# Kernel optimization log

Hardware: AMD Instinct MI355X
Metric: run time of the kernel (lower is better)

## Reference

```python
import jax, jax.numpy as jnp
import numpy as np

Z_DIM = 64
K = 2048
N = 32768


def setup_inputs() -> dict:
    key = jax.random.key(0)
    k1, k2 = jax.random.split(key)
    x = jax.random.normal(k1, (N, Z_DIM), dtype=jnp.float32)
    # init.normal_(locs, std=sqrt(z_dim))
    locs = jax.random.normal(k2, (K, Z_DIM), dtype=jnp.float32) * np.sqrt(Z_DIM)
    logits = jnp.zeros((K,), dtype=jnp.float32)  # maxent buffer
    return {"x": x, "locs": locs, "logits": logits}


def reference(x, locs, logits):
    d = x.shape[-1]
    var = jnp.float32(d)  # scale = sqrt(z_dim) -> variance = z_dim
    # squared distances [N, K] via cdist expansion (avoids [N,K,d] intermediate)
    sq = (
        jnp.sum(x * x, axis=-1, keepdims=True)
        + jnp.sum(locs * locs, axis=-1)[None, :]
        - 2.0 * (x @ locs.T)
    )
    # Independent Normal log prob summed over z_dim
    log_norm_const = d * (0.5 * jnp.log(2.0 * jnp.pi) + 0.5 * jnp.log(var))
    comp_log_prob = -0.5 * sq / var - log_norm_const  # [N, K]
    mix_logits = jax.nn.log_softmax(logits)  # Categorical normalizes logits
    wlp = comp_log_prob + mix_logits  # weighted_log_prob, [N, K]
    log_prob = jax.nn.logsumexp(wlp, axis=-1)  # [N]
    modes = jnp.argmax(wlp, axis=-1)  # assign_modes, [N]
    quantized = locs[modes]  # hard_quantize, [N, z_dim]
    return log_prob, quantized
```

## Files before the change

kernel.cpp:

```cpp
#include <hip/hip_runtime.h>
#include <math.h>

#define N_SAMP 32768
#define K_COMP 2048
#define ZD 64
#define LNC 191.896324792608546f
#define LN2F 0.69314718055994531f
#define INV_LN2 1.44269504088896340f
#define S2C 0.02254211001388974f

#define TILES_TOT 128
#define TPS 8
#define STAGES (TILES_TOT / TPS)
#define STAGE_B (TPS * 2048)

typedef __attribute__((ext_vector_type(8))) short short8;
typedef __attribute__((ext_vector_type(4))) float v4f;

#if __has_builtin(__builtin_amdgcn_exp2f)
#define EXP2(x) __builtin_amdgcn_exp2f(x)
#else
#define EXP2(x) exp2f(x)
#endif

typedef const __attribute__((address_space(1))) unsigned int* gas_t;
typedef __attribute__((address_space(3))) unsigned int* las_t;
__device__ inline void gload_lds16(const void* g, void* l) {
    __builtin_amdgcn_global_load_lds((gas_t)g, (las_t)l, 16, 0, 0);
}

__device__ inline unsigned short f2bf(float f) {
    unsigned int u = __float_as_uint(f);
    u += 0x7fffu + ((u >> 16) & 1u);
    return (unsigned short)(u >> 16);
}
__device__ inline float bf2f(unsigned short h) {
    return __uint_as_float(((unsigned int)h) << 16);
}
__device__ inline float med3f(float x, float y, float z) {
    return fmaxf(fminf(x, y), fminf(fmaxf(x, y), z));
}

__global__ __launch_bounds__(256) void prep_kernel(
    const float* __restrict__ locs, const float* __restrict__ logits,
    float* __restrict__ ck2, float* __restrict__ lse_out,
    char* __restrict__ lf) {
    if (blockIdx.x < 64) {
        int gid = blockIdx.x * 256 + threadIdx.x;
        int k = gid >> 3;
        int dc = gid & 7;
        int T = k >> 4, n = k & 15;

        const float* src = locs + (size_t)k * ZD + dc * 8;
        float4 u0 = *(const float4*)(src);
        float4 u1 = *(const float4*)(src + 4);
        float a[8] = {u0.x, u0.y, u0.z, u0.w, u1.x, u1.y, u1.z, u1.w};

        short8 h;
        float sq = 0.f;
#pragma unroll
        for (int j = 0; j < 8; ++j) {
            h[j] = (short)f2bf(a[j]);
            sq = fmaf(a[j], a[j], sq);
        }
        *(short8*)(lf + (size_t)T * 2048 + (dc >> 2) * 1024 +
                   ((size_t)(n + 16 * (dc & 3))) * 16) = h;

        sq += __shfl_xor(sq, 1);
        sq += __shfl_xor(sq, 2);
        sq += __shfl_xor(sq, 4);
        if (dc == 0) ck2[k] = (logits[k] - sq * (1.0f / 128.0f)) * INV_LN2;
    } else {
        __shared__ float red[4];
        int tid = threadIdx.x;
        int wv = tid >> 6, ln = tid & 63;
        float lm = -INFINITY;
        for (int i = tid; i < K_COMP; i += 256) lm = fmaxf(lm, logits[i]);
#pragma unroll
        for (int d = 1; d < 64; d <<= 1) lm = fmaxf(lm, __shfl_xor(lm, d));
        if (ln == 0) red[wv] = lm;
        __syncthreads();
        float M = fmaxf(fmaxf(red[0], red[1]), fmaxf(red[2], red[3]));
        float ls = 0.f;
        for (int i = tid; i < K_COMP; i += 256) ls += __expf(logits[i] - M);
#pragma unroll
        for (int d = 1; d < 64; d <<= 1) ls += __shfl_xor(ls, d);
        __syncthreads();
        if (ln == 0) red[wv] = ls;
        __syncthreads();
        if (tid == 0) *lse_out = M + __logf(red[0] + red[1] + red[2] + red[3]);
    }
}

__global__ __launch_bounds__(256, 2) void mix_kernel(
    const float* __restrict__ x, const float* __restrict__ locs,
    const char* __restrict__ lf, const float* __restrict__ ck2,
    const float* __restrict__ lse_ptr, float* __restrict__ out) {

    __shared__ char buf[2][STAGE_B];
    __shared__ int cb1[64], cb2[64], cb3[64];
    __shared__ int amax_sh[64];

    const int tid  = threadIdx.x;
    const int lane = tid & 63;
    const int wv   = __builtin_amdgcn_readfirstlane(tid >> 6);
    const int n    = lane & 15;
    const int quad = lane >> 4;
    const int sbase = blockIdx.x * 64;
    const int srow  = sbase + wv * 16 + n;

    short8 bh0, bh1, bl0, bl1;
    float xs;
    {
        const float* xp = x + (size_t)srow * ZD + quad * 8;
        float4 u0 = *(const float4*)(xp);
        float4 u1 = *(const float4*)(xp + 4);
        float4 u2 = *(const float4*)(xp + 32);
        float4 u3 = *(const float4*)(xp + 36);
        float a[8] = {u0.x, u0.y, u0.z, u0.w, u1.x, u1.y, u1.z, u1.w};
        float b[8] = {u2.x, u2.y, u2.z, u2.w, u3.x, u3.y, u3.z, u3.w};
        float p = 0.f;
#pragma unroll
        for (int j = 0; j < 8; ++j) {
            unsigned short h;
            h = f2bf(a[j]); bh0[j] = (short)h; bl0[j] = (short)f2bf(a[j] - bf2f(h));
            h = f2bf(b[j]); bh1[j] = (short)h; bl1[j] = (short)f2bf(b[j] - bf2f(h));
            p = fmaf(a[j], a[j], p);
            p = fmaf(b[j], b[j], p);
        }
        p += __shfl_xor(p, 16);
        p += __shfl_xor(p, 32);
        xs = p;
    }

    const char* gsrc0 = lf + (size_t)wv * 4096 + lane * 16;
    char* ldst0 = &buf[0][wv * 4096];

#define DMA(S, b) do {                                                   \
    const char* _g = gsrc0 + (size_t)(S) * STAGE_B;                      \
    char* _l = ldst0 + (b) * STAGE_B;                                    \
    gload_lds16(_g, _l);                                                 \
    gload_lds16(_g + 1024, _l + 1024);                                   \
    gload_lds16(_g + 2048, _l + 2048);                                   \
    gload_lds16(_g + 3072, _l + 3072);                                   \
} while (0)

    float m1 = -1e30f, m2 = -1e30f, m3 = -1e30f;
    int i1 = 0, i2 = 0, i3 = 0;
    float s0 = 0.f, s1 = 0.f;

    DMA(0, 0);
    __syncthreads();

    for (int S = 0; S < STAGES; ++S) {
        const int b = S & 1;
        if (S + 1 < STAGES) DMA(S + 1, b ^ 1);

        const float* ckS = ck2 + S * (TPS * 16) + quad * 4;
        const char* base = &buf[b][lane * 16];
        const int kb0 = S * (TPS * 16) + quad * 4;

#pragma unroll
        for (int j = 0; j < TPS; ++j) {
            const char* p0 = base + j * 2048;
            short8 a0 = *(const short8*)(p0);
            short8 a1 = *(const short8*)(p0 + 1024);
            float4 cc = *(const float4*)(ckS + j * 16);

            v4f acc = {0.f, 0.f, 0.f, 0.f};
            acc = __builtin_amdgcn_mfma_f32_16x16x32_bf16(a0, bh0, acc, 0, 0, 0);
            acc = __builtin_amdgcn_mfma_f32_16x16x32_bf16(a1, bh1, acc, 0, 0, 0);
            acc = __builtin_amdgcn_mfma_f32_16x16x32_bf16(a0, bl0, acc, 0, 0, 0);
            acc = __builtin_amdgcn_mfma_f32_16x16x32_bf16(a1, bl1, acc, 0, 0, 0);

            const int kb = kb0 + j * 16;
            float w0 = fmaf(acc.x, S2C, cc.x);
            float w1 = fmaf(acc.y, S2C, cc.y);
            float w2 = fmaf(acc.z, S2C, cc.z);
            float w3 = fmaf(acc.w, S2C, cc.w);
            s0 += EXP2(w0) + EXP2(w1);
            s1 += EXP2(w2) + EXP2(w3);

            float T4 = fmaxf(fmaxf(w0, w1), fmaxf(w2, w3));
            bool c = T4 > m1;
            float z = fminf(T4, m1);
            int zi = c ? i1 : kb;
            m1 = fmaxf(T4, m1);
            i1 = c ? kb : i1;
            float m3old = m3;
            bool c2 = z > m2;
            m3 = med3f(z, m2, m3);
            i3 = c2 ? i2 : ((z > m3old) ? zi : i3);
            m2 = fmaxf(z, m2);
            i2 = c2 ? zi : i2;
        }
        __syncthreads();
    }

    float sum = s0 + s1;
#pragma unroll
    for (int d = 16; d <= 32; d <<= 1) {
        sum += __shfl_xor(sum, d);
        float M1 = __shfl_xor(m1, d), M2 = __shfl_xor(m2, d), M3 = __shfl_xor(m3, d);
        int   I1 = __shfl_xor(i1, d), I2 = __shfl_xor(i2, d), I3 = __shfl_xor(i3, d);
        bool cc = (M1 > m1) || (M1 == m1 && I1 < i1);
        float w2v = cc ? M2 : m2;  int w2i = cc ? I2 : i2;
        float w3v = cc ? M3 : m3;  int w3i = cc ? I3 : i3;
        float lv  = cc ? m1 : M1;  int li  = cc ? i1 : I1;
        float l2v = cc ? m2 : M2;  int l2i = cc ? i2 : I2;
        m1 = cc ? M1 : m1;  i1 = cc ? I1 : i1;
        bool c2 = lv > w2v;
        float nm2 = c2 ? lv : w2v;  int ni2 = c2 ? li : w2i;
        float z3 = c2 ? w2v : lv;   int zi3 = c2 ? w2i : li;
        float nm3 = fmaxf(z3, fmaxf(w3v, l2v));
        int ni3 = (z3 >= w3v && z3 >= l2v) ? zi3 : ((w3v >= l2v) ? w3i : l2i);
        m2 = nm2; i2 = ni2; m3 = nm3; i3 = ni3;
    }

    if (quad == 0) {
        float bias = -xs * (1.0f / 128.0f) - LNC;
        out[srow] = fmaf(__log2f(sum), LN2F, bias - lse_ptr[0]);
        int s = wv * 16 + n;
        cb1[s] = i1; cb2[s] = i2; cb3[s] = i3;
    }
    __syncthreads();

    {
        int s = tid >> 2;
        int jj = tid & 3;
        const float4* xrow = (const float4*)(x + (size_t)(sbase + s) * ZD);
        float bestv = -1e30f;
        int bestk = 0x7fffffff;
        int bases[3] = {cb1[s], cb2[s], cb3[s]};
#pragma unroll
        for (int ci = 0; ci < 3; ++ci) {
            int k = bases[ci] + jj;
            const float4* lrow = (const float4*)(locs + (size_t)k * ZD);
            float dot = 0.f;
#pragma unroll
            for (int dd = 0; dd < 16; ++dd) {
                float4 xv = xrow[dd];
                float4 lv = lrow[dd];
                dot = fmaf(xv.x, lv.x, dot);
                dot = fmaf(xv.y, lv.y, dot);
                dot = fmaf(xv.z, lv.z, dot);
                dot = fmaf(xv.w, lv.w, dot);
            }
            float v = fmaf(dot, S2C, ck2[k]);
            if (v > bestv || (v == bestv && k < bestk)) { bestv = v; bestk = k; }
        }
#pragma unroll
        for (int d = 1; d <= 2; d <<= 1) {
            float ov = __shfl_xor(bestv, d);
            int   ok = __shfl_xor(bestk, d);
            if (ov > bestv || (ov == bestv && ok < bestk)) { bestv = ov; bestk = ok; }
        }
        if (jj == 0) amax_sh[s] = bestk;
    }
    __syncthreads();

    const float4* lq = (const float4*)locs;
    float4* oq = (float4*)(out + N_SAMP + (size_t)sbase * ZD);
#pragma unroll
    for (int i = tid; i < 64 * (ZD / 4); i += 256) {
        int r = i >> 4, c = i & 15;
        oq[i] = lq[(size_t)amax_sh[r] * (ZD / 4) + c];
    }
#undef DMA
}

extern "C" void kernel_launch(void* const* d_in, const int* in_sizes, int n_in,
                              void* d_out, int out_size, void* d_ws, size_t ws_size,
                              hipStream_t stream) {
    const float* x      = (const float*)d_in[0];
    const float* locs   = (const float*)d_in[1];
    const float* logits = (const float*)d_in[2];
    float* out = (float*)d_out;

    float* ck2 = (float*)d_ws;
    float* lse = (float*)((char*)d_ws + 8192);
    char*  lf  = (char*)d_ws + 16384;

    prep_kernel<<<65, 256, 0, stream>>>(locs, logits, ck2, lse, lf);
    mix_kernel<<<N_SAMP / 64, 256, 0, stream>>>(x, locs, lf, ck2, lse, out);
}
```

Baseline: 118.4 us.

## Split component range across two wave groups per block with cross-group top-3 merge

Doubles the block to 512 threads, with two groups of four waves each scanning half of the 2048 components for the same 64 samples. Per-group sums and top-3 candidates go through shared memory and are merged before the fp32 rescoring. The inner loop now interleaves two independent MFMA accumulation chains, and the top-3 insertion is rewritten as a simpler compare-select. This aims to raise wave-level parallelism and MFMA ILP, at the cost of an extra sync and merge step and heavier register and occupancy pressure (launch bounds 512,4).

Result: faster. 106.0 us (-10.5%).

```diff
diff --git a/kernel.cpp b/kernel.cpp
--- a/kernel.cpp
+++ b/kernel.cpp
@@ -9,10 +9,8 @@
 #define INV_LN2 1.44269504088896340f
 #define S2C 0.02254211001388974f
 
-#define TILES_TOT 128
-#define TPS 8
-#define STAGES (TILES_TOT / TPS)
-#define STAGE_B (TPS * 2048)
+#define STAGES 16
+#define STAGE_B 16384
 
 typedef __attribute__((ext_vector_type(8))) short short8;
 typedef __attribute__((ext_vector_type(4))) float v4f;
@@ -36,9 +34,6 @@
 }
 __device__ inline float bf2f(unsigned short h) {
     return __uint_as_float(((unsigned int)h) << 16);
-}
-__device__ inline float med3f(float x, float y, float z) {
-    return fmaxf(fminf(x, y), fminf(fmaxf(x, y), z));
 }
 
 __global__ __launch_bounds__(256) void prep_kernel(
@@ -92,25 +87,29 @@
     }
 }
 
-__global__ __launch_bounds__(256, 2) void mix_kernel(
+__global__ __launch_bounds__(512, 4) void mix_kernel(
     const float* __restrict__ x, const float* __restrict__ locs,
     const char* __restrict__ lf, const float* __restrict__ ck2,
     const float* __restrict__ lse_ptr, float* __restrict__ out) {
 
     __shared__ char buf[2][STAGE_B];
-    __shared__ int cb1[64], cb2[64], cb3[64];
-    __shared__ int amax_sh[64];
+    __shared__ float wm1[2][64], wm2[2][64], wm3[2][64], wsum[2][64];
+    __shared__ int   wi1[2][64], wi2[2][64], wi3[2][64];
+    __shared__ float xsq_sh[64];
+    __shared__ int   cb[3][64];
+    __shared__ int   amax_sh[64];
 
     const int tid  = threadIdx.x;
     const int lane = tid & 63;
     const int wv   = __builtin_amdgcn_readfirstlane(tid >> 6);
+    const int sg   = __builtin_amdgcn_readfirstlane(wv & 3);
+    const int kg   = __builtin_amdgcn_readfirstlane(wv >> 2);
     const int n    = lane & 15;
     const int quad = lane >> 4;
     const int sbase = blockIdx.x * 64;
-    const int srow  = sbase + wv * 16 + n;
+    const int srow  = sbase + sg * 16 + n;
 
     short8 bh0, bh1, bl0, bl1;
-    float xs;
     {
         const float* xp = x + (size_t)srow * ZD + quad * 8;
         float4 u0 = *(const float4*)(xp);
@@ -130,25 +129,41 @@
         }
         p += __shfl_xor(p, 16);
         p += __shfl_xor(p, 32);
-        xs = p;
-    }
-
-    const char* gsrc0 = lf + (size_t)wv * 4096 + lane * 16;
-    char* ldst0 = &buf[0][wv * 4096];
+        if (kg == 0 && quad == 0) xsq_sh[sg * 16 + n] = p;
+    }
+
+    const char* gsrc0 = lf + (size_t)((wv >> 2) * 64 + (wv & 3)) * 2048 + lane * 16;
+    char* ldst0 = &buf[0][wv * 2048];
 
 #define DMA(S, b) do {                                                   \
-    const char* _g = gsrc0 + (size_t)(S) * STAGE_B;                      \
+    const char* _g = gsrc0 + (size_t)(S) * (4 * 2048);                   \
     char* _l = ldst0 + (b) * STAGE_B;                                    \
     gload_lds16(_g, _l);                                                 \
     gload_lds16(_g + 1024, _l + 1024);                                   \
-    gload_lds16(_g + 2048, _l + 2048);                                   \
-    gload_lds16(_g + 3072, _l + 3072);                                   \
 } while (0)
 
     float m1 = -1e30f, m2 = -1e30f, m3 = -1e30f;
     int i1 = 0, i2 = 0, i3 = 0;
     float s0 = 0.f, s1 = 0.f;
 
+#define INS(v, kb) do {                                                  \
+    bool c1 = (v) > m1, c2 = (v) > m2, c3 = (v) > m3;                    \
+    m3 = c2 ? m2 : (c3 ? (v) : m3);  i3 = c2 ? i2 : (c3 ? (kb) : i3);    \
+    m2 = c1 ? m1 : (c2 ? (v) : m2);  i2 = c1 ? i1 : (c2 ? (kb) : i2);    \
+    m1 = c1 ? (v) : m1;              i1 = c1 ? (kb) : i1;                \
+} while (0)
+
+#define EPI(acc, cc, kb) do {                                            \
+    float w0 = fmaf((acc).x, S2C, (cc).x);                               \
+    float w1 = fmaf((acc).y, S2C, (cc).y);                               \
+    float w2 = fmaf((acc).z, S2C, (cc).z);                               \
+    float w3 = fmaf((acc).w, S2C, (cc).w);                               \
+    s0 += EXP2(w0) + EXP2(w1);                                           \
+    s1 += EXP2(w2) + EXP2(w3);                                           \
+    float v4 = fmaxf(fmaxf(w0, w1), fmaxf(w2, w3));                      \
+    INS(v4, kb);                                                         \
+} while (0)
+
     DMA(0, 0);
     __syncthreads();
 
@@ -156,43 +171,35 @@
         const int b = S & 1;
         if (S + 1 < STAGES) DMA(S + 1, b ^ 1);
 
-        const float* ckS = ck2 + S * (TPS * 16) + quad * 4;
-        const char* base = &buf[b][lane * 16];
-        const int kb0 = S * (TPS * 16) + quad * 4;
-
-#pragma unroll
-        for (int j = 0; j < TPS; ++j) {
-            const char* p0 = base + j * 2048;
-            short8 a0 = *(const short8*)(p0);
-            short8 a1 = *(const short8*)(p0 + 1024);
-            float4 cc = *(const float4*)(ckS + j * 16);
-
-            v4f acc = {0.f, 0.f, 0.f, 0.f};
-            acc = __builtin_amdgcn_mfma_f32_16x16x32_bf16(a0, bh0, acc, 0, 0, 0);
-            acc = __builtin_amdgcn_mfma_f32_16x16x32_bf16(a1, bh1, acc, 0, 0, 0);
-            acc = __builtin_amdgcn_mfma_f32_16x16x32_bf16(a0, bl0, acc, 0, 0, 0);
-            acc = __builtin_amdgcn_mfma_f32_16x16x32_bf16(a1, bl1, acc, 0, 0, 0);
-
-            const int kb = kb0 + j * 16;
-            float w0 = fmaf(acc.x, S2C, cc.x);
-            float w1 = fmaf(acc.y, S2C, cc.y);
-            float w2 = fmaf(acc.z, S2C, cc.z);
-            float w3 = fmaf(acc.w, S2C, cc.w);
-            s0 += EXP2(w0) + EXP2(w1);
-            s1 += EXP2(w2) + EXP2(w3);
-
-            float T4 = fmaxf(fmaxf(w0, w1), fmaxf(w2, w3));
-            bool c = T4 > m1;
-            float z = fminf(T4, m1);
-            int zi = c ? i1 : kb;
-            m1 = fmaxf(T4, m1);
-            i1 = c ? kb : i1;
-            float m3old = m3;
-            bool c2 = z > m2;
-            m3 = med3f(z, m2, m3);
-            i3 = c2 ? i2 : ((z > m3old) ? zi : i3);
-            m2 = fmaxf(z, m2);
-            i2 = c2 ? zi : i2;
+        const int tb = kg * 64 + 4 * S;
+        const float* ckS = ck2 + tb * 16 + quad * 4;
+        const char* base = &buf[b][(kg * 4) * 2048 + lane * 16];
+        const int kb0 = tb * 16 + quad * 4;
+
+#pragma unroll
+        for (int jp = 0; jp < 4; jp += 2) {
+            const char* p0 = base + jp * 2048;
+            const char* p1 = p0 + 2048;
+            short8 a00 = *(const short8*)(p0);
+            short8 a01 = *(const short8*)(p0 + 1024);
+            short8 a10 = *(const short8*)(p1);
+            short8 a11 = *(const short8*)(p1 + 1024);
+            float4 cc0 = *(const float4*)(ckS + jp * 16);
+            float4 cc1 = *(const float4*)(ckS + jp * 16 + 16);
+
+            v4f ca = {0.f, 0.f, 0.f, 0.f};
+            v4f cb2_ = {0.f, 0.f, 0.f, 0.f};
+            ca   = __builtin_amdgcn_mfma_f32_16x16x32_bf16(a00, bh0, ca, 0, 0, 0);
+            cb2_ = __builtin_amdgcn_mfma_f32_16x16x32_bf16(a10, bh0, cb2_, 0, 0, 0);
+            ca   = __builtin_amdgcn_mfma_f32_16x16x32_bf16(a01, bh1, ca, 0, 0, 0);
+            cb2_ = __builtin_amdgcn_mfma_f32_16x16x32_bf16(a11, bh1, cb2_, 0, 0, 0);
+            ca   = __builtin_amdgcn_mfma_f32_16x16x32_bf16(a00, bl0, ca, 0, 0, 0);
+            cb2_ = __builtin_amdgcn_mfma_f32_16x16x32_bf16(a10, bl0, cb2_, 0, 0, 0);
+            ca   = __builtin_amdgcn_mfma_f32_16x16x32_bf16(a01, bl1, ca, 0, 0, 0);
+            cb2_ = __builtin_amdgcn_mfma_f32_16x16x32_bf16(a11, bl1, cb2_, 0, 0, 0);
+
+            EPI(ca,   cc0, kb0 + jp * 16);
+            EPI(cb2_, cc1, kb0 + jp * 16 + 16);
         }
         __syncthreads();
     }
@@ -203,38 +210,38 @@
         sum += __shfl_xor(sum, d);
         float M1 = __shfl_xor(m1, d), M2 = __shfl_xor(m2, d), M3 = __shfl_xor(m3, d);
         int   I1 = __shfl_xor(i1, d), I2 = __shfl_xor(i2, d), I3 = __shfl_xor(i3, d);
-        bool cc = (M1 > m1) || (M1 == m1 && I1 < i1);
-        float w2v = cc ? M2 : m2;  int w2i = cc ? I2 : i2;
-        float w3v = cc ? M3 : m3;  int w3i = cc ? I3 : i3;
-        float lv  = cc ? m1 : M1;  int li  = cc ? i1 : I1;
-        float l2v = cc ? m2 : M2;  int l2i = cc ? i2 : I2;
-        m1 = cc ? M1 : m1;  i1 = cc ? I1 : i1;
-        bool c2 = lv > w2v;
-        float nm2 = c2 ? lv : w2v;  int ni2 = c2 ? li : w2i;
-        float z3 = c2 ? w2v : lv;   int zi3 = c2 ? w2i : li;
-        float nm3 = fmaxf(z3, fmaxf(w3v, l2v));
-        int ni3 = (z3 >= w3v && z3 >= l2v) ? zi3 : ((w3v >= l2v) ? w3i : l2i);
-        m2 = nm2; i2 = ni2; m3 = nm3; i3 = ni3;
-    }
-
+        INS(M1, I1); INS(M2, I2); INS(M3, I3);
+    }
     if (quad == 0) {
-        float bias = -xs * (1.0f / 128.0f) - LNC;
-        out[srow] = fmaf(__log2f(sum), LN2F, bias - lse_ptr[0]);
-        int s = wv * 16 + n;
-        cb1[s] = i1; cb2[s] = i2; cb3[s] = i3;
+        int s = sg * 16 + n;
+        wm1[kg][s] = m1; wm2[kg][s] = m2; wm3[kg][s] = m3;
+        wi1[kg][s] = i1; wi2[kg][s] = i2; wi3[kg][s] = i3;
+        wsum[kg][s] = sum;
+    }
+    __syncthreads();
+
+    if (tid < 64) {
+        float m1 = wm1[0][tid], m2 = wm2[0][tid], m3 = wm3[0][tid];
+        int   i1 = wi1[0][tid], i2 = wi2[0][tid], i3 = wi3[0][tid];
+        INS(wm1[1][tid], wi1[1][tid]);
+        INS(wm2[1][tid], wi2[1][tid]);
+        INS(wm3[1][tid], wi3[1][tid]);
+        float S = wsum[0][tid] + wsum[1][tid];
+        float bias = -xsq_sh[tid] * (1.0f / 128.0f) - LNC;
+        out[sbase + tid] = fmaf(__log2f(S), LN2F, bias - lse_ptr[0]);
+        cb[0][tid] = i1; cb[1][tid] = i2; cb[2][tid] = i3;
     }
     __syncthreads();
 
     {
-        int s = tid >> 2;
-        int jj = tid & 3;
+        int s = tid >> 3;
+        int j = tid & 7;
         const float4* xrow = (const float4*)(x + (size_t)(sbase + s) * ZD);
         float bestv = -1e30f;
         int bestk = 0x7fffffff;
-        int bases[3] = {cb1[s], cb2[s], cb3[s]};
-#pragma unroll
-        for (int ci = 0; ci < 3; ++ci) {
-            int k = bases[ci] + jj;
+#pragma unroll
+        for (int ci = j; ci < 12; ci += 8) {
+            int k = cb[ci >> 2][s] + (ci & 3);
             const float4* lrow = (const float4*)(locs + (size_t)k * ZD);
             float dot = 0.f;
 #pragma unroll
@@ -250,23 +257,25 @@
             if (v > bestv || (v == bestv && k < bestk)) { bestv = v; bestk = k; }
         }
 #pragma unroll
-        for (int d = 1; d <= 2; d <<= 1) {
+        for (int d = 1; d <= 4; d <<= 1) {
             float ov = __shfl_xor(bestv, d);
             int   ok = __shfl_xor(bestk, d);
             if (ov > bestv || (ov == bestv && ok < bestk)) { bestv = ov; bestk = ok; }
         }
-        if (jj == 0) amax_sh[s] = bestk;
+        if (j == 0) amax_sh[s] = bestk;
     }
     __syncthreads();
 
     const float4* lq = (const float4*)locs;
     float4* oq = (float4*)(out + N_SAMP + (size_t)sbase * ZD);
 #pragma unroll
-    for (int i = tid; i < 64 * (ZD / 4); i += 256) {
+    for (int i = tid; i < 64 * (ZD / 4); i += 512) {
         int r = i >> 4, c = i & 15;
         oq[i] = lq[(size_t)amax_sh[r] * (ZD / 4) + c];
     }
 #undef DMA
+#undef INS
+#undef EPI
 }
 
 extern "C" void kernel_launch(void* const* d_in, const int* in_sizes, int n_in,
@@ -282,5 +291,5 @@
     char*  lf  = (char*)d_ws + 16384;
 
     prep_kernel<<<65, 256, 0, stream>>>(locs, logits, ck2, lse, lf);
-    mix_kernel<<<N_SAMP / 64, 256, 0, stream>>>(x, locs, lf, ck2, lse, out);
-}
+    mix_kernel<<<N_SAMP / 64, 512, 0, stream>>>(x, locs, lf, ck2, lse, out);
+}
```
